# Optimization experiments

Hardware: AMD Instinct MI355X
Metric: run time of the kernel (lower is better)

## Reference

```python
import jax, jax.numpy as jnp
import numpy as np

B, N, FIN, H, D = 8, 2048, 64, 4, 32
ALPHA = 0.2  # LeakyReLU negative slope


def setup_inputs() -> dict:
    key = jax.random.key(0)
    k1, k2, k3, k4 = jax.random.split(key, 4)
    h = jax.random.normal(k1, (B, N, FIN), dtype=jnp.float32)
    adj = jax.random.randint(k2, (B, N, N), 0, 2).astype(jnp.int32)
    # ensure self-loops so every softmax row has at least one unmasked entry
    idx = jnp.arange(N)
    adj = adj.at[:, idx, idx].set(1)
    W = jax.random.normal(k3, (FIN, H * D), dtype=jnp.float32) * 0.1
    a = jax.random.normal(k4, (H, 2 * D), dtype=jnp.float32) * 0.1
    return {"h": h, "adj": adj, "W": W, "a": a}


def reference(h, adj, W, a):
    # h: (B,N,Fin), adj: (B,N,N) int, W: (Fin,H*D), a: (H,2D)
    Bn, Nn, _ = h.shape
    Hh, twoD = a.shape
    Dd = twoD // 2
    Wh = (h @ W).reshape(Bn, Nn, Hh, Dd).transpose(0, 2, 1, 3)  # (B,H,N,D)
    # e_ij = leakyrelu(Wh_i . a1 + Wh_j . a2) -- avoids O(N^2 * 2D) concat
    src = jnp.einsum('bhnd,hd->bhn', Wh, a[:, :Dd])  # (B,H,N)
    dst = jnp.einsum('bhnd,hd->bhn', Wh, a[:, Dd:])  # (B,H,N)
    e = jax.nn.leaky_relu(src[:, :, :, None] + dst[:, :, None, :], negative_slope=ALPHA)  # (B,H,N,N)
    e = jnp.where(adj[:, None, :, :] == 0, -jnp.inf, e)
    attn = jax.nn.softmax(e, axis=-1)  # (B,H,N,N)
    out = jnp.einsum('bhij,bhjd->bhid', attn, Wh)  # (B,H,N,D)
    return out.transpose(0, 2, 1, 3).reshape(Bn, Nn, Hh * Dd)
```

## Files before the change

kernel.cpp:

```cpp
#include <hip/hip_runtime.h>

typedef short short8 __attribute__((ext_vector_type(8)));
typedef _Float16 half8 __attribute__((ext_vector_type(8)));
typedef _Float16 half2v __attribute__((ext_vector_type(2)));
typedef float floatx4 __attribute__((ext_vector_type(4)));

extern "C" __device__ _Float16 __ocml_exp2_f16(_Float16);

#define B_   8
#define N_   2048
#define FIN_ 64
#define H_   4
#define D_   32
#define HD_  128
#define ALPHA_ 0.2f
#define LOG2E_ 1.4426950408889634f


__global__ __launch_bounds__(256) void gat_prep4(
    const float* __restrict__ h, const float* __restrict__ W, const float* __restrict__ a,
    unsigned short* __restrict__ WhF, float* __restrict__ src, unsigned short* __restrict__ dstb)
{
    __shared__ float Ws[FIN_][HD_];
    __shared__ float hsT[FIN_][36];
    int bx = blockIdx.x;
    int b = bx >> 6;
    int n0 = (bx & 63) * 32;
    int tid = threadIdx.x;

    #pragma unroll
    for (int it = 0; it < 8; ++it) {
        int idx = it * 256 + tid;
        int k = idx >> 5, c4 = (idx & 31) << 2;
        *(float4*)&Ws[k][c4] = *(const float4*)&W[k * HD_ + c4];
    }
    #pragma unroll
    for (int it = 0; it < 8; ++it) {
        int idx = it * 256 + tid;
        int r = idx >> 6, k = idx & 63;
        hsT[k][r] = h[((size_t)b * N_ + n0 + r) * FIN_ + k];
    }
    __syncthreads();

    int c = tid & 127;
    int rq = tid >> 7;
    int hh = c >> 5, d = c & 31;
    float acc[16];
    #pragma unroll
    for (int r = 0; r < 16; ++r) acc[r] = 0.f;
    for (int k = 0; k < FIN_; ++k) {
        float wv = Ws[k][c];
        float4 h0 = *(const float4*)&hsT[k][rq * 16];
        float4 h1 = *(const float4*)&hsT[k][rq * 16 + 4];
        float4 h2 = *(const float4*)&hsT[k][rq * 16 + 8];
        float4 h3 = *(const float4*)&hsT[k][rq * 16 + 12];
        acc[0]  += h0.x * wv; acc[1]  += h0.y * wv; acc[2]  += h0.z * wv; acc[3]  += h0.w * wv;
        acc[4]  += h1.x * wv; acc[5]  += h1.y * wv; acc[6]  += h1.z * wv; acc[7]  += h1.w * wv;
        acc[8]  += h2.x * wv; acc[9]  += h2.y * wv; acc[10] += h2.z * wv; acc[11] += h2.w * wv;
        acc[12] += h3.x * wv; acc[13] += h3.y * wv; acc[14] += h3.z * wv; acc[15] += h3.w * wv;
    }

    {
        int half = d >> 4, n = d & 15;
        int j0 = n0 + rq * 16;
        int it0 = j0 >> 5;
        int g0 = (j0 >> 3) & 3;
        #pragma unroll
        for (int rr = 0; rr < 2; ++rr) {
            __attribute__((aligned(16))) unsigned pk4[4];
            #pragma unroll
            for (int q = 0; q < 4; ++q)
                pk4[q] = __builtin_bit_cast(unsigned,
                    __builtin_amdgcn_cvt_pkrtz(acc[rr * 8 + 2 * q], acc[rr * 8 + 2 * q + 1]));
            size_t fi = ((((size_t)b * H_ + hh) * 64 + it0) * 2 + half) * 64
                        + (size_t)(g0 + rr) * 16 + n;
            *(uint4*)&WhF[fi * 8] = *(uint4*)pk4;
        }
    }

    float a1v = a[hh * 64 + d];
    float a2v = a[hh * 64 + 32 + d];
    #pragma unroll
    for (int r = 0; r < 16; ++r) {
        float s1 = acc[r] * a1v;
        float s2 = acc[r] * a2v;
        #pragma unroll
        for (int off = 16; off >= 1; off >>= 1) {
            s1 += __shfl_xor(s1, off, 32);
            s2 += __shfl_xor(s2, off, 32);
        }
        if (d == 0) {
            int n = n0 + rq * 16 + r;
            src[(b * H_ + hh) * N_ + n] = s1 * LOG2E_;
            _Float16 hv = (_Float16)(s2 * LOG2E_);
            dstb[(b * H_ + hh) * N_ + n] = __builtin_bit_cast(unsigned short, hv);
        }
    }
}

__global__ __launch_bounds__(256, 6) void gat_main15(
    const int* __restrict__ adj, const unsigned short* __restrict__ WhF,
    const float* __restrict__ src, const unsigned short* __restrict__ dstb,
    float* __restrict__ out)
{
    __shared__ unsigned adjW[16][72];

    int bx = blockIdx.x;
    int b  = bx >> 7;
    int i0 = (bx & 127) * 16;
    int tid = threadIdx.x;
    int wv = tid >> 6, l = tid & 63;

    const int* adjBase = adj + ((size_t)(b * N_ + i0 + wv * 4)) * N_ + l;

    int vals[16];
    #pragma unroll
    for (int rr = 0; rr < 4; ++rr)
        #pragma unroll
        for (int cc = 0; cc < 4; ++cc)
            vals[rr * 4 + cc] = adjBase[rr * N_ + cc * 64];

    int h = wv, g = l >> 4, m = l & 15;
    int g8 = g << 3;
    _Float16 sv = (_Float16)src[(b * H_ + h) * N_ + i0 + m];
    half2v s2; s2[0] = sv; s2[1] = sv;
    const _Float16 alf = (_Float16)0.2f;
    const unsigned short* WhB =
        WhF + ((size_t)(b * H_ + h) * 64) * 1024 + l * 8;
    const unsigned short* dstG = dstb + (size_t)(b * H_ + h) * N_;

    short8 onesS;
    #pragma unroll
    for (int q = 0; q < 8; ++q) onesS[q] = (short)0x3C00;
    half8 ones = __builtin_bit_cast(half8, onesS);

    floatx4 acc0 = {0.f, 0.f, 0.f, 0.f};
    floatx4 acc1 = {0.f, 0.f, 0.f, 0.f};
    floatx4 acc2 = {0.f, 0.f, 0.f, 0.f};

    short8 bf0_a = *(const short8*)&WhB[0];
    short8 bf1_a = *(const short8*)&WhB[512];
    short8 bf0_b = *(const short8*)&WhB[1024];
    short8 bf1_b = *(const short8*)&WhB[1536];
    uint4 dv_a = *(const uint4*)&dstG[g8];
    uint4 dv_b = *(const uint4*)&dstG[32 + g8];

    for (int q = 0; q < 8; ++q) {
        #pragma unroll
        for (int rr = 0; rr < 4; ++rr)
            #pragma unroll
            for (int cc = 0; cc < 4; ++cc) {
                unsigned long long mk = __ballot(vals[rr * 4 + cc] != 0);
                if (l == 0)
                    *(unsigned long long*)&adjW[wv * 4 + rr][2 * (q * 4 + cc)] = mk;
            }
        __syncthreads();

        uint4 shv0 = *(const uint4*)&adjW[m][q * 8];
        uint4 shv1 = *(const uint4*)&adjW[m][q * 8 + 4];

        if (q < 7) {
            #pragma unroll
            for (int rr = 0; rr < 4; ++rr)
                #pragma unroll
                for (int cc = 0; cc < 4; ++cc)
                    vals[rr * 4 + cc] = adjBase[rr * N_ + (q + 1) * 256 + cc * 64];
        }

        #pragma unroll
        for (int jj = 0; jj < 8; ++jj) {
            int it = q * 8 + jj;
            int fn = (it + 2) * 1024;
            short8 bf0_n = *(const short8*)&WhB[fn];
            short8 bf1_n = *(const short8*)&WhB[fn + 512];
            int j2 = ((it + 2) << 5) + g8;
            uint4  dv_n = *(const uint4*)&dstG[(j2 < N_) ? j2 : g8];

            unsigned sh = (jj < 4 ? ((const unsigned*)&shv0)[jj]
                                  : ((const unsigned*)&shv1)[jj - 4]) >> g8;
            const unsigned* du = (const unsigned*)&dv_a;
            __attribute__((aligned(16))) unsigned pk[4];
            #pragma unroll
            for (int c2 = 0; c2 < 4; ++c2) {
                half2v d2 = __builtin_bit_cast(half2v, du[c2]);
                half2v e2 = s2 + d2;
                half2v t2 = e2 * alf;
                e2 = __builtin_elementwise_max(e2, t2);
                half2v x2;
                x2[0] = __ocml_exp2_f16(e2[0]);
                x2[1] = __ocml_exp2_f16(e2[1]);
                unsigned mk = ((((sh >> (2 * c2 + 1)) & 1u) << 16)
                               | ((sh >> (2 * c2)) & 1u)) * 0x3C00u;
                x2 = x2 * __builtin_bit_cast(half2v, mk);
                pk[c2] = __builtin_bit_cast(unsigned, x2);
            }
            half8 af = __builtin_bit_cast(half8, *(uint4*)pk);
            acc0 = __builtin_amdgcn_mfma_f32_16x16x32_f16(
                       af, __builtin_bit_cast(half8, bf0_a), acc0, 0, 0, 0);
            acc1 = __builtin_amdgcn_mfma_f32_16x16x32_f16(
                       af, __builtin_bit_cast(half8, bf1_a), acc1, 0, 0, 0);
            acc2 = __builtin_amdgcn_mfma_f32_16x16x32_f16(af, ones, acc2, 0, 0, 0);
            bf0_a = bf0_b; bf0_b = bf0_n;
            bf1_a = bf1_b; bf1_b = bf1_n;
            dv_a = dv_b;   dv_b = dv_n;
        }
    }

    #pragma unroll
    for (int r = 0; r < 4; ++r) {
        float inv = 1.f / acc2[r];
        size_t o = ((size_t)b * N_ + i0 + g * 4 + r) * HD_ + h * 32 + m;
        out[o]      = acc0[r] * inv;
        out[o + 16] = acc1[r] * inv;
    }
}

extern "C" void kernel_launch(void* const* d_in, const int* in_sizes, int n_in,
                              void* d_out, int out_size, void* d_ws, size_t ws_size,
                              hipStream_t stream) {
    const float* h   = (const float*)d_in[0];
    const int*   adj = (const int*)d_in[1];
    const float* W   = (const float*)d_in[2];
    const float* a   = (const float*)d_in[3];
    float* out = (float*)d_out;

    unsigned short* WhF  = (unsigned short*)d_ws;
    float*          src  = (float*)((char*)d_ws + 4u * 1024 * 1024);
    unsigned short* dstb = (unsigned short*)((char*)d_ws + 4u * 1024 * 1024 + 256u * 1024);

    gat_prep4<<<B_ * (N_ / 32), 256, 0, stream>>>(h, W, a, WhF, src, dstb);
    gat_main15<<<B_ * (N_ / 16), 256, 0, stream>>>(adj, WhF, src, dstb, out);
}
```

Measured before the change: 227.1 us.

## Read adjacency per lane as additive mask, drop ballot staging and barriers

Each wave now loads its 16x32 adjacency tile straight from global memory with vector int4 loads, software-pipelined two iterations ahead. It turns each entry into an additive fp16 -inf or 0 term before the LeakyReLU and exp2. This replaces the ballot bitmask built in shared memory and the per-chunk __syncthreads, so the main loop becomes one flat 64-iteration loop with no block barriers. The dst logits are also staged into shared memory, and the occupancy hint drops from 6 to 4 blocks per CU. In exchange, all four head-waves fetch the same adjacency rows, so L1/L2 traffic rises about fourfold, and the mask trick assumes adjacency values are exactly 0 or 1.

```diff
diff --git a/kernel.cpp b/kernel.cpp
--- a/kernel.cpp
+++ b/kernel.cpp
@@ -98,12 +98,12 @@
     }
 }
 
-__global__ __launch_bounds__(256, 6) void gat_main15(
+__global__ __launch_bounds__(256, 4) void gat_main20(
     const int* __restrict__ adj, const unsigned short* __restrict__ WhF,
     const float* __restrict__ src, const unsigned short* __restrict__ dstb,
     float* __restrict__ out)
 {
-    __shared__ unsigned adjW[16][72];
+    __shared__ unsigned short dsts[H_][N_];
 
     int bx = blockIdx.x;
     int b  = bx >> 7;
@@ -111,23 +111,25 @@
     int tid = threadIdx.x;
     int wv = tid >> 6, l = tid & 63;
 
-    const int* adjBase = adj + ((size_t)(b * N_ + i0 + wv * 4)) * N_ + l;
-
-    int vals[16];
-    #pragma unroll
-    for (int rr = 0; rr < 4; ++rr)
-        #pragma unroll
-        for (int cc = 0; cc < 4; ++cc)
-            vals[rr * 4 + cc] = adjBase[rr * N_ + cc * 64];
-
     int h = wv, g = l >> 4, m = l & 15;
     int g8 = g << 3;
+
+    {
+        const unsigned short* dsrcW = dstb + (size_t)(b * H_ + h) * N_;
+        #pragma unroll
+        for (int it = 0; it < 4; ++it)
+            *(uint4*)&dsts[h][it * 512 + l * 8] =
+                *(const uint4*)&dsrcW[it * 512 + l * 8];
+    }
+
+    const int* adjP = adj + ((size_t)(b * N_ + i0 + m)) * N_ + g8;
+
     _Float16 sv = (_Float16)src[(b * H_ + h) * N_ + i0 + m];
     half2v s2; s2[0] = sv; s2[1] = sv;
     const _Float16 alf = (_Float16)0.2f;
     const unsigned short* WhB =
         WhF + ((size_t)(b * H_ + h) * 64) * 1024 + l * 8;
-    const unsigned short* dstG = dstb + (size_t)(b * H_ + h) * N_;
+    const unsigned short* dstH = &dsts[h][0];
 
     short8 onesS;
     #pragma unroll
@@ -138,72 +140,64 @@
     floatx4 acc1 = {0.f, 0.f, 0.f, 0.f};
     floatx4 acc2 = {0.f, 0.f, 0.f, 0.f};
 
+    int4 a0_a = *(const int4*)&adjP[0];
+    int4 a1_a = *(const int4*)&adjP[4];
+    int4 a0_b = *(const int4*)&adjP[32];
+    int4 a1_b = *(const int4*)&adjP[36];
     short8 bf0_a = *(const short8*)&WhB[0];
     short8 bf1_a = *(const short8*)&WhB[512];
     short8 bf0_b = *(const short8*)&WhB[1024];
     short8 bf1_b = *(const short8*)&WhB[1536];
-    uint4 dv_a = *(const uint4*)&dstG[g8];
-    uint4 dv_b = *(const uint4*)&dstG[32 + g8];
-
-    for (int q = 0; q < 8; ++q) {
-        #pragma unroll
-        for (int rr = 0; rr < 4; ++rr)
-            #pragma unroll
-            for (int cc = 0; cc < 4; ++cc) {
-                unsigned long long mk = __ballot(vals[rr * 4 + cc] != 0);
-                if (l == 0)
-                    *(unsigned long long*)&adjW[wv * 4 + rr][2 * (q * 4 + cc)] = mk;
-            }
-        __syncthreads();
-
-        uint4 shv0 = *(const uint4*)&adjW[m][q * 8];
-        uint4 shv1 = *(const uint4*)&adjW[m][q * 8 + 4];
-
-        if (q < 7) {
-            #pragma unroll
-            for (int rr = 0; rr < 4; ++rr)
-                #pragma unroll
-                for (int cc = 0; cc < 4; ++cc)
-                    vals[rr * 4 + cc] = adjBase[rr * N_ + (q + 1) * 256 + cc * 64];
-        }
-
-        #pragma unroll
-        for (int jj = 0; jj < 8; ++jj) {
-            int it = q * 8 + jj;
-            int fn = (it + 2) * 1024;
-            short8 bf0_n = *(const short8*)&WhB[fn];
-            short8 bf1_n = *(const short8*)&WhB[fn + 512];
-            int j2 = ((it + 2) << 5) + g8;
-            uint4  dv_n = *(const uint4*)&dstG[(j2 < N_) ? j2 : g8];
-
-            unsigned sh = (jj < 4 ? ((const unsigned*)&shv0)[jj]
-                                  : ((const unsigned*)&shv1)[jj - 4]) >> g8;
-            const unsigned* du = (const unsigned*)&dv_a;
-            __attribute__((aligned(16))) unsigned pk[4];
-            #pragma unroll
-            for (int c2 = 0; c2 < 4; ++c2) {
-                half2v d2 = __builtin_bit_cast(half2v, du[c2]);
-                half2v e2 = s2 + d2;
-                half2v t2 = e2 * alf;
-                e2 = __builtin_elementwise_max(e2, t2);
-                half2v x2;
-                x2[0] = __ocml_exp2_f16(e2[0]);
-                x2[1] = __ocml_exp2_f16(e2[1]);
-                unsigned mk = ((((sh >> (2 * c2 + 1)) & 1u) << 16)
-                               | ((sh >> (2 * c2)) & 1u)) * 0x3C00u;
-                x2 = x2 * __builtin_bit_cast(half2v, mk);
-                pk[c2] = __builtin_bit_cast(unsigned, x2);
-            }
-            half8 af = __builtin_bit_cast(half8, *(uint4*)pk);
-            acc0 = __builtin_amdgcn_mfma_f32_16x16x32_f16(
-                       af, __builtin_bit_cast(half8, bf0_a), acc0, 0, 0, 0);
-            acc1 = __builtin_amdgcn_mfma_f32_16x16x32_f16(
-                       af, __builtin_bit_cast(half8, bf1_a), acc1, 0, 0, 0);
-            acc2 = __builtin_amdgcn_mfma_f32_16x16x32_f16(af, ones, acc2, 0, 0, 0);
-            bf0_a = bf0_b; bf0_b = bf0_n;
-            bf1_a = bf1_b; bf1_b = bf1_n;
-            dv_a = dv_b;   dv_b = dv_n;
-        }
+    uint4 dv_a = *(const uint4*)&dstH[g8];
+    uint4 dv_b = *(const uint4*)&dstH[32 + g8];
+
+    auto mkpair = [](int px, int py) -> unsigned {
+        unsigned t = ((unsigned)px | ((unsigned)py << 16)) ^ 0x00010001u;
+        return t * 0xFC00u;
+    };
+
+    #pragma unroll 4
+    for (int it = 0; it < 64; ++it) {
+        int itp = (it + 2 < 64) ? (it + 2) : 63;
+        int4 a0_n = *(const int4*)&adjP[itp * 32];
+        int4 a1_n = *(const int4*)&adjP[itp * 32 + 4];
+        int fn = (it + 2) * 1024;
+        short8 bf0_n = *(const short8*)&WhB[fn];
+        short8 bf1_n = *(const short8*)&WhB[fn + 512];
+        int j2 = ((it + 2) << 5) + g8;
+        uint4  dv_n = *(const uint4*)&dstH[(j2 < N_) ? j2 : g8];
+
+        unsigned mk[4];
+        mk[0] = mkpair(a0_a.x, a0_a.y);
+        mk[1] = mkpair(a0_a.z, a0_a.w);
+        mk[2] = mkpair(a1_a.x, a1_a.y);
+        mk[3] = mkpair(a1_a.z, a1_a.w);
+
+        const unsigned* du = (const unsigned*)&dv_a;
+        __attribute__((aligned(16))) unsigned pk[4];
+        #pragma unroll
+        for (int c2 = 0; c2 < 4; ++c2) {
+            half2v d2 = __builtin_bit_cast(half2v, du[c2]);
+            half2v e2 = s2 + d2;
+            e2 = e2 + __builtin_bit_cast(half2v, mk[c2]);
+            half2v t2 = e2 * alf;
+            e2 = __builtin_elementwise_max(e2, t2);
+            half2v x2;
+            x2[0] = __ocml_exp2_f16(e2[0]);
+            x2[1] = __ocml_exp2_f16(e2[1]);
+            pk[c2] = __builtin_bit_cast(unsigned, x2);
+        }
+        half8 af = __builtin_bit_cast(half8, *(uint4*)pk);
+        acc0 = __builtin_amdgcn_mfma_f32_16x16x32_f16(
+                   af, __builtin_bit_cast(half8, bf0_a), acc0, 0, 0, 0);
+        acc1 = __builtin_amdgcn_mfma_f32_16x16x32_f16(
+                   af, __builtin_bit_cast(half8, bf1_a), acc1, 0, 0, 0);
+        acc2 = __builtin_amdgcn_mfma_f32_16x16x32_f16(af, ones, acc2, 0, 0, 0);
+        a0_a = a0_b; a0_b = a0_n;
+        a1_a = a1_b; a1_b = a1_n;
+        bf0_a = bf0_b; bf0_b = bf0_n;
+        bf1_a = bf1_b; bf1_b = bf1_n;
+        dv_a = dv_b;   dv_b = dv_n;
     }
 
     #pragma unroll
@@ -229,5 +223,5 @@
     unsigned short* dstb = (unsigned short*)((char*)d_ws + 4u * 1024 * 1024 + 256u * 1024);
 
     gat_prep4<<<B_ * (N_ / 32), 256, 0, stream>>>(h, W, a, WhF, src, dstb);
-    gat_main15<<<B_ * (N_ / 16), 256, 0, stream>>>(adj, WhF, src, dstb, out);
+    gat_main20<<<B_ * (N_ / 16), 256, 0, stream>>>(adj, WhF, src, dstb, out);
 }
```

After: 252.6 us. +11.2%, slower.
